# Kernel tuning notes

Measured on AMD Instinct MI355X. Metric: run time of the kernel, lower is better.

Reference implementation:

```python
import jax, jax.numpy as jnp
import numpy as np

NUM_HEADS = 8
NUM_POINTS = 4


def _grid_sample_bilinear(img, grid, H, W):
    """torch F.grid_sample(mode='bilinear', padding='zeros', align_corners=False).
    img:  [B, H, W, D]   grid: [B, S, 2] with (x, y) in [-1, 1].
    Returns [B, S, D].
    """
    gx, gy = grid[..., 0], grid[..., 1]
    # align_corners=False pixel mapping
    x = ((gx + 1.0) * W - 1.0) * 0.5
    y = ((gy + 1.0) * H - 1.0) * 0.5
    x0 = jnp.floor(x)
    y0 = jnp.floor(y)
    wx1 = x - x0
    wy1 = y - y0
    x0i = x0.astype(jnp.int32)
    y0i = y0.astype(jnp.int32)
    img_flat = img.reshape(img.shape[0], H * W, img.shape[-1])  # [B, N, D]

    def corner(xi, yi, w):
        valid = (xi >= 0) & (xi < W) & (yi >= 0) & (yi < H)  # zeros padding
        idx = jnp.clip(yi, 0, H - 1) * W + jnp.clip(xi, 0, W - 1)  # [B, S]
        v = jnp.take_along_axis(img_flat, idx[..., None], axis=1)  # [B, S, D]
        return v * (w * valid.astype(img.dtype))[..., None]

    out = corner(x0i, y0i, (1.0 - wx1) * (1.0 - wy1))
    out += corner(x0i + 1, y0i, wx1 * (1.0 - wy1))
    out += corner(x0i, y0i + 1, (1.0 - wx1) * wy1)
    out += corner(x0i + 1, y0i + 1, wx1 * wy1)
    return out


def setup_inputs() -> dict:
    key = jax.random.key(0)
    ks = jax.random.split(key, 12)
    B, Q, D = 4, 1024, 256
    H, W = 128, 128
    nh, npts = NUM_HEADS, NUM_POINTS
    f32 = jnp.float32
    return {
        "query": jax.random.normal(ks[0], (B, Q, D), f32),
        "reference_points": jax.random.uniform(ks[1], (B, Q, 2), f32),
        "value": jax.random.normal(ks[2], (B, H * W, D), f32),
        "W_off": jax.random.normal(ks[3], (D, nh * npts * 2), f32) * 0.02,
        "b_off": jax.random.normal(ks[4], (nh * npts * 2,), f32) * 0.02,
        "W_attn": jax.random.normal(ks[5], (D, nh * npts), f32) * 0.02,
        "b_attn": jax.random.normal(ks[6], (nh * npts,), f32) * 0.02,
        "W_v": jax.random.normal(ks[7], (D, D), f32) * (D ** -0.5),
        "b_v": jnp.zeros((D,), f32),
        "W_out": jax.random.normal(ks[8], (nh * D, D), f32) * ((nh * D) ** -0.5),
        "b_out": jnp.zeros((D,), f32),
        "H": H,
        "W": W,
    }


def reference(query, reference_points, value, W_off, b_off, W_attn, b_attn,
              W_v, b_v, W_out, b_out, H, W):
    B, Q, D = query.shape
    nh, npts = NUM_HEADS, NUM_POINTS
    # learned offsets and per-point attention weights
    offsets = (query @ W_off + b_off).reshape(B, Q, nh, npts, 2)
    attn = jax.nn.softmax((query @ W_attn + b_attn).reshape(B, Q, nh, npts), axis=-1)
    # sampling locations in [-1, 1]
    locs = reference_points[:, :, None, None, :] + offsets * 0.1
    locs = jnp.clip(locs, 0.0, 1.0) * 2.0 - 1.0
    # value projection -> 2D feature map [B, H, W, D]
    img = (value @ W_v + b_v).reshape(B, H, W, D)
    # sample all heads/points at once
    grid = locs.reshape(B, Q * nh * npts, 2)
    sampled = _grid_sample_bilinear(img, grid, H, W).reshape(B, Q, nh, npts, D)
    # weighted reduce over points, concat heads
    weighted = jnp.einsum("bqhpd,bqhp->bqhd", sampled, attn)
    out = weighted.reshape(B, Q, nh * D) @ W_out + b_out
    return out
```

## Files before the change

### kernel.cpp

```cpp
#include <hip/hip_runtime.h>
#include <hip/hip_bf16.h>
#include <math.h>

constexpr int B  = 4;
constexpr int Q  = 1024;
constexpr int D  = 256;
constexpr int NH = 8;
constexpr int NP = 4;
constexpr int H  = 128;
constexpr int W  = 128;
constexpr int HW = H * W;
constexpr int KAUG = 2112;

typedef short   bf16x8  __attribute__((ext_vector_type(8)));
typedef float   f32x4   __attribute__((ext_vector_type(4)));
typedef short   short4v __attribute__((ext_vector_type(4)));
typedef unsigned short ushort8v __attribute__((ext_vector_type(8)));

__device__ inline unsigned short f2bf(float f) {
    union { float f; unsigned u; } v; v.f = f;
    unsigned r = v.u + 0x7fff + ((v.u >> 16) & 1);
    return (unsigned short)(r >> 16);
}
__device__ inline float bf2f(unsigned short s) {
    union { unsigned u; float f; } v; v.u = ((unsigned)s) << 16;
    return v.f;
}

__device__ inline void async16(const void* g, void* l) {
    __builtin_amdgcn_global_load_lds(
        (const __attribute__((address_space(1))) unsigned*)g,
        (__attribute__((address_space(3))) unsigned*)l, 16, 0, 0);
}

template <int OUTMODE>
__device__ __forceinline__ void gemm64_body(
        unsigned short* __restrict__ lds,
        const unsigned short* __restrict__ A, int lda,
        const unsigned short* __restrict__ Bt, int ldb,
        const float* __restrict__ bias,
        void* __restrict__ Cout, int ldc, int K,
        int m0, int n0, int zblk) {
    const int tid  = threadIdx.x;
    const int lane = tid & 63;
    const int w    = tid >> 6;
    const int wm   = w >> 1, wn = w & 1;
    if (OUTMODE == 1) Bt += (size_t)zblk * 256;

    const int srow = w * 8 + (lane >> 3);
    const int schk = (lane & 7) ^ (lane >> 3);
    const unsigned short* ag0 = A  + (size_t)(m0 + srow)      * lda + schk * 8;
    const unsigned short* ag1 = A  + (size_t)(m0 + srow + 32) * lda + schk * 8;
    const unsigned short* bg0 = Bt + (size_t)(n0 + srow)      * ldb + schk * 8;
    const unsigned short* bg1 = Bt + (size_t)(n0 + srow + 32) * ldb + schk * 8;
    const int l0 = w * 512 + lane * 8;
    const int l1 = l0 + 2048;

    int aoff[2][2], boff[2][2];
    #pragma unroll
    for (int i = 0; i < 2; ++i)
        #pragma unroll
        for (int kk = 0; kk < 2; ++kk) {
            const int ar = wm * 32 + i * 16 + (lane & 15);
            aoff[i][kk] = ar * 64 + ((((lane >> 4) + kk * 4) ^ (ar & 7)) * 8);
            const int br = wn * 32 + i * 16 + (lane & 15);
            boff[i][kk] = br * 64 + ((((lane >> 4) + kk * 4) ^ (br & 7)) * 8);
        }

    f32x4 acc[2][2];
    #pragma unroll
    for (int i = 0; i < 2; ++i)
        #pragma unroll
        for (int j = 0; j < 2; ++j) acc[i][j] = (f32x4){0.f, 0.f, 0.f, 0.f};

    async16(ag0, &lds[0 * 4096 + l0]); async16(ag1, &lds[0 * 4096 + l1]);
    async16(bg0, &lds[1 * 4096 + l0]); async16(bg1, &lds[1 * 4096 + l1]);

    const int niter = K >> 6;
    for (int it = 0; it < niter; ++it) {
        __syncthreads();
        const int cur = (it & 1) * 2;
        if (it + 1 < niter) {
            const int nxt = 2 - cur;
            const int ko  = (it + 1) * 64;
            async16(ag0 + ko, &lds[nxt * 4096 + l0]);
            async16(ag1 + ko, &lds[nxt * 4096 + l1]);
            async16(bg0 + ko, &lds[(nxt + 1) * 4096 + l0]);
            async16(bg1 + ko, &lds[(nxt + 1) * 4096 + l1]);
        }
        bf16x8 af[2][2], bfv[2][2];
        #pragma unroll
        for (int i = 0; i < 2; ++i)
            #pragma unroll
            for (int kk = 0; kk < 2; ++kk) {
                af[i][kk]  = *(const bf16x8*)&lds[cur * 4096 + aoff[i][kk]];
                bfv[i][kk] = *(const bf16x8*)&lds[(cur + 1) * 4096 + boff[i][kk]];
            }
        #pragma unroll
        for (int i = 0; i < 2; ++i)
            #pragma unroll
            for (int j = 0; j < 2; ++j)
                #pragma unroll
                for (int kk = 0; kk < 2; ++kk)
                    acc[i][j] = __builtin_amdgcn_mfma_f32_16x16x32_bf16(
                        af[i][kk], bfv[j][kk], acc[i][j], 0, 0, 0);
    }

    const int colb = n0 + wn * 32 + (lane & 15);
    const int rowb = m0 + wm * 32 + (lane >> 4) * 4;
    if (OUTMODE == 0) {
        float* C = (float*)Cout;
        #pragma unroll
        for (int j = 0; j < 2; ++j) {
            const int col = colb + j * 16;
            const float bb = bias[col];
            #pragma unroll
            for (int i = 0; i < 2; ++i)
                #pragma unroll
                for (int r = 0; r < 4; ++r)
                    C[(size_t)(rowb + i * 16 + r) * ldc + col] = acc[i][j][r] + bb;
        }
    } else {
        unsigned short* Wt = (unsigned short*)Cout;
        const int ocol = zblk * 256;
        #pragma unroll
        for (int j = 0; j < 2; ++j) {
            const int col = colb + j * 16;
            #pragma unroll
            for (int i = 0; i < 2; ++i)
                #pragma unroll
                for (int r = 0; r < 4; ++r)
                    Wt[(size_t)col * ldc + ocol + rowb + i * 16 + r] =
                        f2bf(acc[i][j][r]);
        }
    }
}

constexpr int R1_CONV = 0;
constexpr int R1_SG   = R1_CONV + (B * HW * D) / 1024;
constexpr int R1_WOUT = R1_SG   + 128;
constexpr int R1_WV   = R1_WOUT + (NH * D * D) / 256;
constexpr int R1_BV   = R1_WV   + (D * D) / 1024;
constexpr int R1_END  = R1_BV   + (D * 64) / 256;

__global__ __launch_bounds__(256)
void k_stage1(const float* __restrict__ value,
              const float* __restrict__ query,
              const float* __restrict__ W_off,  const float* __restrict__ b_off,
              const float* __restrict__ W_attn, const float* __restrict__ b_attn,
              const float* __restrict__ b_v,    const float* __restrict__ W_out,
              const float* __restrict__ W_v,
              unsigned short* __restrict__ val_bf,
              float* __restrict__ raw,
              unsigned short* __restrict__ Wout_t,
              unsigned short* __restrict__ Wv_bf,
              unsigned short* __restrict__ WcT) {
    __shared__ __align__(16) float smem[2][16][68];
    const int blk = blockIdx.x;
    const int tid = threadIdx.x;

    if (blk < R1_SG) {
        const int i = (blk * 1024) + tid * 4;
        const float4 v = *(const float4*)&value[i];
        short4v o;
        o.x = (short)f2bf(v.x); o.y = (short)f2bf(v.y);
        o.z = (short)f2bf(v.z); o.w = (short)f2bf(v.w);
        *(short4v*)&val_bf[i] = o;
    } else if (blk < R1_WOUT) {
        const int blkr = blk - R1_SG;
        const int m0 = (blkr >> 1) * 64;
        const int n0 = (blkr & 1) * 64;
        float (*As)[68] = smem[0];
        float (*Bs)[68] = smem[1];
        const int t  = tid;
        const int tx = t & 15, ty = t >> 4;
        const int arow = t >> 2, akg = (t & 3) * 4;
        const int brow = t >> 4, bcol = (t & 15) * 4;

        float acc[4][4] = {};
        for (int k0 = 0; k0 < D; k0 += 16) {
            const float4 av = *(const float4*)&query[(size_t)(m0 + arow) * D + k0 + akg];
            const int kr = k0 + brow;
            const int j  = n0 + bcol;
            float4 bv;
            if (j < 64)      bv = *(const float4*)&W_off[kr * 64 + j];
            else if (j < 96) bv = *(const float4*)&W_attn[kr * 32 + (j - 64)];
            else             bv = (float4){0.f, 0.f, 0.f, 0.f};
            __syncthreads();
            As[akg + 0][arow] = av.x;
            As[akg + 1][arow] = av.y;
            As[akg + 2][arow] = av.z;
            As[akg + 3][arow] = av.w;
            *(float4*)&Bs[brow][bcol] = bv;
            __syncthreads();
            #pragma unroll
            for (int kk = 0; kk < 16; ++kk) {
                const float4 a = *(const float4*)&As[kk][ty * 4];
                const float4 b = *(const float4*)&Bs[kk][tx * 4];
                acc[0][0] += a.x * b.x; acc[0][1] += a.x * b.y; acc[0][2] += a.x * b.z; acc[0][3] += a.x * b.w;
                acc[1][0] += a.y * b.x; acc[1][1] += a.y * b.y; acc[1][2] += a.y * b.z; acc[1][3] += a.y * b.w;
                acc[2][0] += a.z * b.x; acc[2][1] += a.z * b.y; acc[2][2] += a.z * b.z; acc[2][3] += a.z * b.w;
                acc[3][0] += a.w * b.x; acc[3][1] += a.w * b.y; acc[3][2] += a.w * b.z; acc[3][3] += a.w * b.w;
            }
        }
        float bb[4];
        #pragma unroll
        for (int c = 0; c < 4; ++c) {
            const int col = n0 + tx * 4 + c;
            bb[c] = (col < 64) ? b_off[col] : ((col < 96) ? b_attn[col - 64] : 0.0f);
        }
        #pragma unroll
        for (int i = 0; i < 4; ++i) {
            const int m = m0 + ty * 4 + i;
            float4 r;
            r.x = acc[i][0] + bb[0];
            r.y = acc[i][1] + bb[1];
            r.z = acc[i][2] + bb[2];
            r.w = acc[i][3] + bb[3];
            *(float4*)&raw[(size_t)m * 128 + n0 + tx * 4] = r;
        }
    } else if (blk < R1_WV) {
        const int i = (blk - R1_WOUT) * 256 + tid;
        const int n = i >> 11, k = i & 2047;
        Wout_t[i] = f2bf(W_out[(size_t)k * D + n]);
    } else if (blk < R1_BV) {
        const int i = (blk - R1_WV) * 1024 + tid * 4;
        const float4 v = *(const float4*)&W_v[i];
        short4v o;
        o.x = (short)f2bf(v.x); o.y = (short)f2bf(v.y);
        o.z = (short)f2bf(v.z); o.w = (short)f2bf(v.w);
        *(short4v*)&Wv_bf[i] = o;
    } else {
        const int t = (blk - R1_BV) * 256 + tid;
        const int n = t >> 6, c = t & 63;
        float v = 0.0f;
        if (c < 8) {
            #pragma unroll 8
            for (int j = 0; j < D; ++j)
                v += b_v[j] * W_out[((size_t)c * D + j) * D + n];
        }
        WcT[(size_t)n * KAUG + 2048 + c] = f2bf(v);
    }
}

constexpr int R2_WC  = B * Q;
constexpr int R2_END = R2_WC + 128;

__global__ __launch_bounds__(256)
void k_stage2(const unsigned short* __restrict__ val,
              const float* __restrict__ raw,
              const float* __restrict__ refpts,
              const unsigned short* __restrict__ Wv_bf,
              const unsigned short* __restrict__ Wout_t,
              unsigned short* __restrict__ sv,
              unsigned short* __restrict__ WcT) {
    __shared__ __align__(16) unsigned short smem[16384];
    const int blk = blockIdx.x;
    const int tid = threadIdx.x;

    if (blk >= R2_WC) {
        const int blkr = blk - R2_WC;
        const int z  = blkr >> 4;
        const int m0 = ((blkr >> 2) & 3) * 64;
        const int n0 = (blkr & 3) * 64;
        gemm64_body<1>(smem, Wv_bf, D, Wout_t, NH * D, nullptr, WcT, KAUG, D,
                       m0, n0, z);
        return;
    }

    const int bq   = blk;
    const int b    = bq >> 10;
    const int lane = tid & 63;
    const int w    = tid >> 6;

    float* s_raw = (float*)smem;
    int*   s_off = (int*)((char*)smem + 512);
    float* s_wgt = (float*)((char*)smem + 1024);

    if (tid < 128) s_raw[tid] = raw[(size_t)bq * 128 + tid];
    __syncthreads();

    if (tid < NH * NP) {
        const int h = tid >> 2;
        float m = -1e30f;
        #pragma unroll
        for (int p = 0; p < NP; ++p) m = fmaxf(m, s_raw[64 + h * 4 + p]);
        float s = 0.0f;
        #pragma unroll
        for (int p = 0; p < NP; ++p) s += __expf(s_raw[64 + h * 4 + p] - m);
        const float a = __expf(s_raw[64 + tid] - m) / s;

        const float refx = refpts[(size_t)bq * 2 + 0];
        const float refy = refpts[(size_t)bq * 2 + 1];
        const float gx = fminf(fmaxf(refx + s_raw[tid * 2 + 0] * 0.1f, 0.0f), 1.0f) * 2.0f - 1.0f;
        const float gy = fminf(fmaxf(refy + s_raw[tid * 2 + 1] * 0.1f, 0.0f), 1.0f) * 2.0f - 1.0f;
        const float x  = ((gx + 1.0f) * (float)W - 1.0f) * 0.5f;
        const float y  = ((gy + 1.0f) * (float)H - 1.0f) * 0.5f;
        const float x0f = floorf(x), y0f = floorf(y);
        const float wx1 = x - x0f,  wy1 = y - y0f;
        const float wx0 = 1.0f - wx1, wy0 = 1.0f - wy1;
        const int x0 = (int)x0f, y0 = (int)y0f;
        const int x1 = x0 + 1,  y1 = y0 + 1;
        const float vx0 = (x0 >= 0 && x0 < W) ? 1.0f : 0.0f;
        const float vx1 = (x1 >= 0 && x1 < W) ? 1.0f : 0.0f;
        const float vy0 = (y0 >= 0 && y0 < H) ? 1.0f : 0.0f;
        const float vy1 = (y1 >= 0 && y1 < H) ? 1.0f : 0.0f;
        const int xc0 = min(max(x0, 0), W - 1);
        const int xc1 = min(max(x1, 0), W - 1);
        const int yc0 = min(max(y0, 0), H - 1);
        const int yc1 = min(max(y1, 0), H - 1);
        s_off[tid * 4 + 0] = yc0 * W + xc0;
        s_off[tid * 4 + 1] = yc0 * W + xc1;
        s_off[tid * 4 + 2] = yc1 * W + xc0;
        s_off[tid * 4 + 3] = yc1 * W + xc1;
        s_wgt[tid * 4 + 0] = a * wx0 * wy0 * vx0 * vy0;
        s_wgt[tid * 4 + 1] = a * wx1 * wy0 * vx1 * vy0;
        s_wgt[tid * 4 + 2] = a * wx0 * wy1 * vx0 * vy1;
        s_wgt[tid * 4 + 3] = a * wx1 * wy1 * vx1 * vy1;
    }
    __syncthreads();

    if (tid < 8) {
        float S = 0.0f;
        #pragma unroll
        for (int c = 0; c < 16; ++c) S += s_wgt[tid * 16 + c];
        sv[(size_t)bq * KAUG + 2048 + tid] = f2bf(S);
    } else if (tid < 64) {
        sv[(size_t)bq * KAUG + 2048 + tid] = 0;
    }

    const int half = lane >> 5;
    const int l5   = lane & 31;
    const unsigned short* ib = val + (size_t)b * HW * D + l5 * 8;

    float acc[2][8] = {};
    #pragma unroll
    for (int g = 0; g < 2; ++g) {
        ushort8v vb[8];
        float    wg[8];
        #pragma unroll
        for (int j = 0; j < 8; ++j) {
            const int flat = w * 32 + (g * 8 + j) * 2 + half;
            wg[j] = s_wgt[flat];
            vb[j] = *(const ushort8v*)(ib + (size_t)s_off[flat] * D);
        }
        #pragma unroll
        for (int j = 0; j < 8; ++j)
            #pragma unroll
            for (int k = 0; k < 8; ++k)
                acc[g][k] += wg[j] * bf2f(vb[j][k]);
    }

    #pragma unroll
    for (int hh = 0; hh < 2; ++hh) {
        float comb[8];
        #pragma unroll
        for (int k = 0; k < 8; ++k)
            comb[k] = acc[hh][k] + __shfl_xor(acc[hh][k], 32, 64);
        if (half == 0) {
            const int h = w * 2 + hh;
            ushort8v o;
            #pragma unroll
            for (int k = 0; k < 8; ++k) o[k] = f2bf(comb[k]);
            *(ushort8v*)&sv[(size_t)bq * KAUG + h * D + l5 * 8] = o;
        }
    }
}

__global__ __launch_bounds__(256)
void k_stage3(const unsigned short* __restrict__ sv,
              const unsigned short* __restrict__ WcT,
              const float* __restrict__ b_out,
              float* __restrict__ out) {
    __shared__ __align__(16) unsigned short smem[16384];
    gemm64_body<0>(smem, sv, KAUG, WcT, KAUG, b_out, out, D, KAUG,
                   blockIdx.x * 64, blockIdx.y * 64, 0);
}

extern "C" void kernel_launch(void* const* d_in, const int* in_sizes, int n_in,
                              void* d_out, int out_size, void* d_ws, size_t ws_size,
                              hipStream_t stream) {
    const float* query  = (const float*)d_in[0];
    const float* refpts = (const float*)d_in[1];
    const float* value  = (const float*)d_in[2];
    const float* W_off  = (const float*)d_in[3];
    const float* b_off  = (const float*)d_in[4];
    const float* W_attn = (const float*)d_in[5];
    const float* b_attn = (const float*)d_in[6];
    const float* W_v    = (const float*)d_in[7];
    const float* b_v    = (const float*)d_in[8];
    const float* W_out  = (const float*)d_in[9];
    const float* b_out  = (const float*)d_in[10];
    float* out = (float*)d_out;

    char* wsb = (char*)d_ws;
    unsigned short* val_bf  = (unsigned short*)(wsb);
    unsigned short* sv      = (unsigned short*)(wsb + 33554432);
    unsigned short* WcT     = (unsigned short*)(wsb + 50855936);
    unsigned short* Wout_t  = (unsigned short*)(wsb + 51937280);
    unsigned short* Wv_bf   = (unsigned short*)(wsb + 52985856);
    float*          raw     = (float*)(wsb + 53116928);

    k_stage1<<<R1_END, 256, 0, stream>>>(value, query, W_off, b_off,
                                         W_attn, b_attn, b_v, W_out, W_v,
                                         val_bf, raw, Wout_t, Wv_bf, WcT);

    k_stage2<<<R2_END, 256, 0, stream>>>(val_bf, raw, refpts, Wv_bf, Wout_t,
                                         sv, WcT);

    {
        dim3 grid((B * Q) / 64, D / 64);
        k_stage3<<<grid, 256, 0, stream>>>(sv, WcT, b_out, out);
    }
}
```

Before: 186.6 us.

## Reorder stage1 blocks, coarsen value conversion, single-buffer WcT GEMM, issue all gathers upfront

Stage 1 now places the small projection and weight-prep blocks first and converts the large value tensor with four float4 chunks per thread, cutting the number of conversion blocks fourfold. The Wv·Wout fold GEMM in stage 2 moves to a single-buffered variant, halving the kernel's static LDS so more sampling blocks can stay resident. The sampling loop now issues all 16 bilinear corner gathers before accumulating, to raise memory-level parallelism at the cost of more live registers.

```diff
diff --git a/kernel.cpp b/kernel.cpp
--- a/kernel.cpp
+++ b/kernel.cpp
@@ -33,19 +33,16 @@
         (__attribute__((address_space(3))) unsigned*)l, 16, 0, 0);
 }
 
-template <int OUTMODE>
-__device__ __forceinline__ void gemm64_body(
+__device__ __forceinline__ void gemm64_dbuf(
         unsigned short* __restrict__ lds,
         const unsigned short* __restrict__ A, int lda,
         const unsigned short* __restrict__ Bt, int ldb,
         const float* __restrict__ bias,
-        void* __restrict__ Cout, int ldc, int K,
-        int m0, int n0, int zblk) {
+        float* __restrict__ C, int ldc, int K, int m0, int n0) {
     const int tid  = threadIdx.x;
     const int lane = tid & 63;
     const int w    = tid >> 6;
     const int wm   = w >> 1, wn = w & 1;
-    if (OUTMODE == 1) Bt += (size_t)zblk * 256;
 
     const int srow = w * 8 + (lane >> 3);
     const int schk = (lane & 7) ^ (lane >> 3);
@@ -108,40 +105,104 @@
 
     const int colb = n0 + wn * 32 + (lane & 15);
     const int rowb = m0 + wm * 32 + (lane >> 4) * 4;
-    if (OUTMODE == 0) {
-        float* C = (float*)Cout;
-        #pragma unroll
-        for (int j = 0; j < 2; ++j) {
-            const int col = colb + j * 16;
-            const float bb = bias[col];
-            #pragma unroll
-            for (int i = 0; i < 2; ++i)
+    #pragma unroll
+    for (int j = 0; j < 2; ++j) {
+        const int col = colb + j * 16;
+        const float bb = bias[col];
+        #pragma unroll
+        for (int i = 0; i < 2; ++i)
+            #pragma unroll
+            for (int r = 0; r < 4; ++r)
+                C[(size_t)(rowb + i * 16 + r) * ldc + col] = acc[i][j][r] + bb;
+    }
+}
+
+__device__ __forceinline__ void gemm64_single_t(
+        unsigned short* __restrict__ lds,
+        const unsigned short* __restrict__ A, int lda,
+        const unsigned short* __restrict__ Bt, int ldb,
+        unsigned short* __restrict__ Wt, int ldc, int K,
+        int m0, int n0, int zblk) {
+    const int tid  = threadIdx.x;
+    const int lane = tid & 63;
+    const int w    = tid >> 6;
+    const int wm   = w >> 1, wn = w & 1;
+    Bt += (size_t)zblk * 256;
+
+    const int srow = w * 8 + (lane >> 3);
+    const int schk = (lane & 7) ^ (lane >> 3);
+    const unsigned short* ag0 = A  + (size_t)(m0 + srow)      * lda + schk * 8;
+    const unsigned short* ag1 = A  + (size_t)(m0 + srow + 32) * lda + schk * 8;
+    const unsigned short* bg0 = Bt + (size_t)(n0 + srow)      * ldb + schk * 8;
+    const unsigned short* bg1 = Bt + (size_t)(n0 + srow + 32) * ldb + schk * 8;
+    const int l0 = w * 512 + lane * 8;
+    const int l1 = l0 + 2048;
+
+    int aoff[2][2], boff[2][2];
+    #pragma unroll
+    for (int i = 0; i < 2; ++i)
+        #pragma unroll
+        for (int kk = 0; kk < 2; ++kk) {
+            const int ar = wm * 32 + i * 16 + (lane & 15);
+            aoff[i][kk] = ar * 64 + ((((lane >> 4) + kk * 4) ^ (ar & 7)) * 8);
+            const int br = wn * 32 + i * 16 + (lane & 15);
+            boff[i][kk] = br * 64 + ((((lane >> 4) + kk * 4) ^ (br & 7)) * 8);
+        }
+
+    f32x4 acc[2][2];
+    #pragma unroll
+    for (int i = 0; i < 2; ++i)
+        #pragma unroll
+        for (int j = 0; j < 2; ++j) acc[i][j] = (f32x4){0.f, 0.f, 0.f, 0.f};
+
+    const int niter = K >> 6;
+    for (int it = 0; it < niter; ++it) {
+        __syncthreads();
+        const int ko = it * 64;
+        async16(ag0 + ko, &lds[l0]);
+        async16(ag1 + ko, &lds[l1]);
+        async16(bg0 + ko, &lds[4096 + l0]);
+        async16(bg1 + ko, &lds[4096 + l1]);
+        __syncthreads();
+        bf16x8 af[2][2], bfv[2][2];
+        #pragma unroll
+        for (int i = 0; i < 2; ++i)
+            #pragma unroll
+            for (int kk = 0; kk < 2; ++kk) {
+                af[i][kk]  = *(const bf16x8*)&lds[aoff[i][kk]];
+                bfv[i][kk] = *(const bf16x8*)&lds[4096 + boff[i][kk]];
+            }
+        #pragma unroll
+        for (int i = 0; i < 2; ++i)
+            #pragma unroll
+            for (int j = 0; j < 2; ++j)
                 #pragma unroll
-                for (int r = 0; r < 4; ++r)
-                    C[(size_t)(rowb + i * 16 + r) * ldc + col] = acc[i][j][r] + bb;
-        }
-    } else {
-        unsigned short* Wt = (unsigned short*)Cout;
-        const int ocol = zblk * 256;
-        #pragma unroll
-        for (int j = 0; j < 2; ++j) {
-            const int col = colb + j * 16;
-            #pragma unroll
-            for (int i = 0; i < 2; ++i)
-                #pragma unroll
-                for (int r = 0; r < 4; ++r)
-                    Wt[(size_t)col * ldc + ocol + rowb + i * 16 + r] =
-                        f2bf(acc[i][j][r]);
-        }
-    }
-}
-
-constexpr int R1_CONV = 0;
-constexpr int R1_SG   = R1_CONV + (B * HW * D) / 1024;
-constexpr int R1_WOUT = R1_SG   + 128;
-constexpr int R1_WV   = R1_WOUT + (NH * D * D) / 256;
-constexpr int R1_BV   = R1_WV   + (D * D) / 1024;
-constexpr int R1_END  = R1_BV   + (D * 64) / 256;
+                for (int kk = 0; kk < 2; ++kk)
+                    acc[i][j] = __builtin_amdgcn_mfma_f32_16x16x32_bf16(
+                        af[i][kk], bfv[j][kk], acc[i][j], 0, 0, 0);
+    }
+
+    const int colb = n0 + wn * 32 + (lane & 15);
+    const int rowb = m0 + wm * 32 + (lane >> 4) * 4;
+    const int ocol = zblk * 256;
+    #pragma unroll
+    for (int j = 0; j < 2; ++j) {
+        const int col = colb + j * 16;
+        #pragma unroll
+        for (int i = 0; i < 2; ++i)
+            #pragma unroll
+            for (int r = 0; r < 4; ++r)
+                Wt[(size_t)col * ldc + ocol + rowb + i * 16 + r] =
+                    f2bf(acc[i][j][r]);
+    }
+}
+
+constexpr int R1_SG   = 0;
+constexpr int R1_BV   = R1_SG   + 128;
+constexpr int R1_WV   = R1_BV   + (D * 64) / 256;
+constexpr int R1_WOUT = R1_WV   + (D * D) / 1024;
+constexpr int R1_CONV = R1_WOUT + (NH * D * D) / 256;
+constexpr int R1_END  = R1_CONV + (B * HW * D) / 4096;
 
 __global__ __launch_bounds__(256)
 void k_stage1(const float* __restrict__ value,
@@ -159,23 +220,14 @@
     const int blk = blockIdx.x;
     const int tid = threadIdx.x;
 
-    if (blk < R1_SG) {
-        const int i = (blk * 1024) + tid * 4;
-        const float4 v = *(const float4*)&value[i];
-        short4v o;
-        o.x = (short)f2bf(v.x); o.y = (short)f2bf(v.y);
-        o.z = (short)f2bf(v.z); o.w = (short)f2bf(v.w);
-        *(short4v*)&val_bf[i] = o;
-    } else if (blk < R1_WOUT) {
-        const int blkr = blk - R1_SG;
-        const int m0 = (blkr >> 1) * 64;
-        const int n0 = (blkr & 1) * 64;
+    if (blk < R1_BV) {
+        const int m0 = (blk >> 1) * 64;
+        const int n0 = (blk & 1) * 64;
         float (*As)[68] = smem[0];
         float (*Bs)[68] = smem[1];
-        const int t  = tid;
-        const int tx = t & 15, ty = t >> 4;
-        const int arow = t >> 2, akg = (t & 3) * 4;
-        const int brow = t >> 4, bcol = (t & 15) * 4;
+        const int tx = tid & 15, ty = tid >> 4;
+        const int arow = tid >> 2, akg = (tid & 3) * 4;
+        const int brow = tid >> 4, bcol = (tid & 15) * 4;
 
         float acc[4][4] = {};
         for (int k0 = 0; k0 < D; k0 += 16) {
@@ -220,17 +272,6 @@
             *(float4*)&raw[(size_t)m * 128 + n0 + tx * 4] = r;
         }
     } else if (blk < R1_WV) {
-        const int i = (blk - R1_WOUT) * 256 + tid;
-        const int n = i >> 11, k = i & 2047;
-        Wout_t[i] = f2bf(W_out[(size_t)k * D + n]);
-    } else if (blk < R1_BV) {
-        const int i = (blk - R1_WV) * 1024 + tid * 4;
-        const float4 v = *(const float4*)&W_v[i];
-        short4v o;
-        o.x = (short)f2bf(v.x); o.y = (short)f2bf(v.y);
-        o.z = (short)f2bf(v.z); o.w = (short)f2bf(v.w);
-        *(short4v*)&Wv_bf[i] = o;
-    } else {
         const int t = (blk - R1_BV) * 256 + tid;
         const int n = t >> 6, c = t & 63;
         float v = 0.0f;
@@ -240,6 +281,28 @@
                 v += b_v[j] * W_out[((size_t)c * D + j) * D + n];
         }
         WcT[(size_t)n * KAUG + 2048 + c] = f2bf(v);
+    } else if (blk < R1_WOUT) {
+        const int i = (blk - R1_WV) * 1024 + tid * 4;
+        const float4 v = *(const float4*)&W_v[i];
+        short4v o;
+        o.x = (short)f2bf(v.x); o.y = (short)f2bf(v.y);
+        o.z = (short)f2bf(v.z); o.w = (short)f2bf(v.w);
+        *(short4v*)&Wv_bf[i] = o;
+    } else if (blk < R1_CONV) {
+        const int i = (blk - R1_WOUT) * 256 + tid;
+        const int n = i >> 11, k = i & 2047;
+        Wout_t[i] = f2bf(W_out[(size_t)k * D + n]);
+    } else {
+        const int base = (blk - R1_CONV) * 4096;
+        #pragma unroll
+        for (int s = 0; s < 4; ++s) {
+            const int i = base + s * 1024 + tid * 4;
+            const float4 v = *(const float4*)&value[i];
+            short4v o;
+            o.x = (short)f2bf(v.x); o.y = (short)f2bf(v.y);
+            o.z = (short)f2bf(v.z); o.w = (short)f2bf(v.w);
+            *(short4v*)&val_bf[i] = o;
+        }
     }
 }
 
@@ -254,7 +317,7 @@
               const unsigned short* __restrict__ Wout_t,
               unsigned short* __restrict__ sv,
               unsigned short* __restrict__ WcT) {
-    __shared__ __align__(16) unsigned short smem[16384];
+    __shared__ __align__(16) unsigned short smem[8192];
     const int blk = blockIdx.x;
     const int tid = threadIdx.x;
 
@@ -263,8 +326,8 @@
         const int z  = blkr >> 4;
         const int m0 = ((blkr >> 2) & 3) * 64;
         const int n0 = (blkr & 3) * 64;
-        gemm64_body<1>(smem, Wv_bf, D, Wout_t, NH * D, nullptr, WcT, KAUG, D,
-                       m0, n0, z);
+        gemm64_single_t(smem, Wv_bf, D, Wout_t, NH * D, WcT, KAUG, D,
+                        m0, n0, z);
         return;
     }
 
@@ -333,22 +396,22 @@
     const int l5   = lane & 31;
     const unsigned short* ib = val + (size_t)b * HW * D + l5 * 8;
 
+    ushort8v vb[16];
+    float    wg[16];
+    #pragma unroll
+    for (int j = 0; j < 16; ++j) {
+        const int flat = w * 32 + j * 2 + half;
+        wg[j] = s_wgt[flat];
+        vb[j] = *(const ushort8v*)(ib + (size_t)s_off[flat] * D);
+    }
+
     float acc[2][8] = {};
     #pragma unroll
-    for (int g = 0; g < 2; ++g) {
-        ushort8v vb[8];
-        float    wg[8];
-        #pragma unroll
-        for (int j = 0; j < 8; ++j) {
-            const int flat = w * 32 + (g * 8 + j) * 2 + half;
-            wg[j] = s_wgt[flat];
-            vb[j] = *(const ushort8v*)(ib + (size_t)s_off[flat] * D);
-        }
-        #pragma unroll
-        for (int j = 0; j < 8; ++j)
-            #pragma unroll
-            for (int k = 0; k < 8; ++k)
-                acc[g][k] += wg[j] * bf2f(vb[j][k]);
+    for (int j = 0; j < 16; ++j) {
+        const int g = j >> 3;
+        #pragma unroll
+        for (int k = 0; k < 8; ++k)
+            acc[g][k] += wg[j] * bf2f(vb[j][k]);
     }
 
     #pragma unroll
@@ -373,8 +436,8 @@
               const float* __restrict__ b_out,
               float* __restrict__ out) {
     __shared__ __align__(16) unsigned short smem[16384];
-    gemm64_body<0>(smem, sv, KAUG, WcT, KAUG, b_out, out, D, KAUG,
-                   blockIdx.x * 64, blockIdx.y * 64, 0);
+    gemm64_dbuf(smem, sv, KAUG, WcT, KAUG, b_out, out, D, KAUG,
+                blockIdx.x * 64, blockIdx.y * 64);
 }
 
 extern "C" void kernel_launch(void* const* d_in, const int* in_sizes, int n_in,
```

Measured after the change: 175.1 us. 6.2% less time.
